# Kernel tuning notes

Measured on AMD Instinct MI355X. Metric: run time of the kernel, lower is better.

The kernel has to match this reference:

```python
import jax, jax.numpy as jnp
import numpy as np

ANCHOR_RADIUS = 5.0


def setup_inputs() -> dict:
    key = jax.random.key(0)
    k1, k2, k3 = jax.random.split(key, 3)
    B, N, E, S = 4, 1024, 32, 2
    embedding = jax.random.normal(k1, (B, N, E), dtype=jnp.float32)
    abs_coords = 10.0 * jax.random.normal(k2, (B, N, S), dtype=jnp.float32)
    patch_mask = jax.random.bernoulli(k3, 0.5, (B, N, N))  # bool [B,N,N]
    return {"embedding": embedding, "abs_coords": abs_coords, "patch_mask": patch_mask}


def reference(embedding, abs_coords, patch_mask):
    B, N, E = embedding.shape
    # pairwise coordinate and embedding differences
    coord_diff = abs_coords[:, :, None, :] - abs_coords[:, None, :, :]   # [B,N,N,2]
    diff = embedding[:, :, None, :] - embedding[:, None, :, :]           # [B,N,N,E]
    diff = diff.at[..., :2].add(coord_diff)
    ssq = jnp.sum(diff * diff, axis=-1)                                   # [B,N,N]
    # safe sqrt: zero grad at zero distance (matches torch norm subgradient)
    dist = jnp.where(ssq == 0, 0.0, jnp.sqrt(jnp.where(ssq == 0, 1.0, ssq)))
    sim = 1.0 - jax.nn.sigmoid(dist * 5.0 / ANCHOR_RADIUS - 5.0)          # [B,N,N]

    # negatives: sim with positive-pair mask and diagonal set to -inf
    eye = jnp.eye(N, dtype=bool)
    neg_mask = patch_mask | eye
    neg_masked = jnp.where(neg_mask, -jnp.inf, sim)                       # [B,N,N]
    lse_neg = jax.scipy.special.logsumexp(neg_masked, axis=-1)            # [B,N]

    # For each positive pair (b,i,j) with patch_mask[b,i,j]:
    #   logits = [sim[b,i,j], neg_masked[b,i,:]] ; CE target=0 ->
    #   loss_contrib = logaddexp(sim[b,i,j], lse_neg[b,i]) - sim[b,i,j]
    lse_tot = jnp.logaddexp(sim, lse_neg[:, :, None])                     # [B,N,N]
    loss = jnp.sum(jnp.where(patch_mask, lse_tot - sim, 0.0))
    return loss
```

## Files before the change

kernel.cpp:

```cpp
#include <hip/hip_runtime.h>

#define BBATCH 4
#define NN 1024
#define EE 32
#define NROW (BBATCH * NN)

typedef short v8s __attribute__((ext_vector_type(8)));
typedef float v4f __attribute__((ext_vector_type(4)));

#define WS_NRM  (NROW * EE * 2)
#define WS_SUM  (WS_NRM + NROW * 4)
#define WS_PART (WS_SUM + NROW * 4)

__device__ __forceinline__ unsigned short f32_to_bf16(float v) {
    unsigned u = __builtin_bit_cast(unsigned, v);
    u += 0x7fffu + ((u >> 16) & 1u);
    return (unsigned short)(u >> 16);
}

__global__ __launch_bounds__(256) void prep_kernel(
    const float* __restrict__ emb, const float* __restrict__ coords,
    unsigned short* __restrict__ yh, float* __restrict__ nrm)
{
    const int idx = blockIdx.x * 256 + threadIdx.x;
    const int g = idx >> 5, e = idx & 31;
    float v = emb[idx];
    if (e < 2) v += coords[g * 2 + e];
    yh[idx] = f32_to_bf16(v);
    float s = v * v;
    #pragma unroll
    for (int off = 16; off > 0; off >>= 1) s += __shfl_xor(s, off, 32);
    if (e == 0) nrm[g] = s;
}

__global__ __launch_bounds__(256) void passA_kernel(
    const unsigned short* __restrict__ yh, const float* __restrict__ nrm,
    const int* __restrict__ mask, float* __restrict__ sums)
{
    const int bid = blockIdx.x;
    const int jg = bid & 3;
    const int is = (bid >> 2) & 63;
    const int b  = bid >> 8;
    const int tid  = threadIdx.x;
    const int wave = tid >> 6, lane = tid & 63;
    const int m = lane & 15, q = lane >> 4;

    const int i0 = is * 16;
    const int rb = b * NN;
    const v8s af = *(const v8s*)(yh + (size_t)(rb + i0 + m) * EE + q * 8);
    float ni[4];
    #pragma unroll
    for (int r = 0; r < 4; ++r) ni[r] = nrm[rb + i0 + q * 4 + r];

    const int jbase = jg * 256 + wave * 64;
    float s[4] = {0.f, 0.f, 0.f, 0.f};

    #pragma unroll
    for (int t = 0; t < 4; ++t) {
        const int j0 = jbase + t * 16;
        const v8s bf = *(const v8s*)(yh + (size_t)(rb + j0 + m) * EE + q * 8);
        const float njv = nrm[rb + j0 + m];
        int mk[4];
        #pragma unroll
        for (int r = 0; r < 4; ++r)
            mk[r] = mask[((size_t)(rb + i0 + q * 4 + r) << 10) + j0 + m];
        v4f d = __builtin_amdgcn_mfma_f32_16x16x32_bf16(af, bf, (v4f){0,0,0,0}, 0, 0, 0);
        #pragma unroll
        for (int r = 0; r < 4; ++r) {
            float ssq  = fmaxf(ni[r] + njv - 2.f * d[r], 0.f);
            float dist = sqrtf(ssq);
            float sim  = 1.f / (1.f + __expf(dist - 5.f));
            bool negm  = (mk[r] != 0) || (i0 + q * 4 + r == j0 + m);
            s[r] += negm ? 0.f : __expf(sim);
        }
    }
    #pragma unroll
    for (int r = 0; r < 4; ++r) {
        float v = s[r];
        #pragma unroll
        for (int off = 8; off > 0; off >>= 1) v += __shfl_down(v, off, 16);
        if (m == 0) atomicAdd(&sums[rb + i0 + q * 4 + r], v);
    }
}

__global__ __launch_bounds__(256) void passB_kernel(
    const unsigned short* __restrict__ yh, const float* __restrict__ nrm,
    const int* __restrict__ mask, const float* __restrict__ sums,
    float* __restrict__ part)
{
    const int bid = blockIdx.x;
    const int jg = bid & 3;
    const int is = (bid >> 2) & 63;
    const int b  = bid >> 8;
    const int tid  = threadIdx.x;
    const int wave = tid >> 6, lane = tid & 63;
    const int m = lane & 15, q = lane >> 4;

    const int i0 = is * 16;
    const int rb = b * NN;
    const v8s af = *(const v8s*)(yh + (size_t)(rb + i0 + m) * EE + q * 8);
    float ni[4], tot[4];
    #pragma unroll
    for (int r = 0; r < 4; ++r) {
        ni[r]  = nrm[rb + i0 + q * 4 + r];
        tot[r] = sums[rb + i0 + q * 4 + r];
    }

    const int jbase = jg * 256 + wave * 64;
    float acc = 0.f;

    #pragma unroll
    for (int t = 0; t < 4; ++t) {
        const int j0 = jbase + t * 16;
        const v8s bf = *(const v8s*)(yh + (size_t)(rb + j0 + m) * EE + q * 8);
        const float njv = nrm[rb + j0 + m];
        int mk[4];
        #pragma unroll
        for (int r = 0; r < 4; ++r)
            mk[r] = mask[((size_t)(rb + i0 + q * 4 + r) << 10) + j0 + m];
        v4f d = __builtin_amdgcn_mfma_f32_16x16x32_bf16(af, bf, (v4f){0,0,0,0}, 0, 0, 0);
        #pragma unroll
        for (int r = 0; r < 4; ++r) {
            float ssq  = fmaxf(ni[r] + njv - 2.f * d[r], 0.f);
            float dist = sqrtf(ssq);
            float sim  = 1.f / (1.f + __expf(dist - 5.f));
            float term = __logf(fmaf(tot[r], __expf(-sim), 1.f));
            acc += (mk[r] != 0) ? term : 0.f;
        }
    }

    __shared__ float wred[4];
    #pragma unroll
    for (int off = 32; off > 0; off >>= 1) acc += __shfl_down(acc, off, 64);
    if (lane == 0) wred[wave] = acc;
    __syncthreads();
    if (tid == 0) part[bid] = wred[0] + wred[1] + wred[2] + wred[3];
}

__global__ __launch_bounds__(256) void reduce_kernel(
    const float* __restrict__ part, float* __restrict__ out)
{
    const int tid = threadIdx.x;
    float s = part[tid] + part[tid + 256] + part[tid + 512] + part[tid + 768];
    #pragma unroll
    for (int off = 32; off > 0; off >>= 1) s += __shfl_down(s, off, 64);
    __shared__ float w[4];
    if ((tid & 63) == 0) w[tid >> 6] = s;
    __syncthreads();
    if (tid == 0) out[0] = w[0] + w[1] + w[2] + w[3];
}

extern "C" void kernel_launch(void* const* d_in, const int* in_sizes, int n_in,
                              void* d_out, int out_size, void* d_ws, size_t ws_size,
                              hipStream_t stream) {
    const float* emb    = (const float*)d_in[0];
    const float* coords = (const float*)d_in[1];
    const int*   mask   = (const int*)d_in[2];

    char* ws = (char*)d_ws;
    unsigned short* yh   = (unsigned short*)ws;
    float*          nrm  = (float*)(ws + WS_NRM);
    float*          sums = (float*)(ws + WS_SUM);
    float*          part = (float*)(ws + WS_PART);

    hipMemsetAsync(sums, 0, NROW * sizeof(float), stream);
    prep_kernel  <<<(NROW * EE) / 256, 256, 0, stream>>>(emb, coords, yh, nrm);
    passA_kernel <<<1024, 256, 0, stream>>>(yh, nrm, mask, sums);
    passB_kernel <<<1024, 256, 0, stream>>>(yh, nrm, mask, sums, part);
    reduce_kernel<<<1, 256, 0, stream>>>(part, (float*)d_out);
}
```

Baseline: 86.88 us.

## Fuse two-pass contrastive loss into one kernel with in-block row sums

Merges passA, passB and the final reduction into one kernel. Each 1024-thread block now owns 16 full rows across all 1024 columns, so the negative-sum for each row is finished in shared memory. The similarity values and mask bits stay in registers for the second phase. This removes the second pass over the mask and MFMA recompute, the per-row atomics and memset, and two kernel launches. The cost is far fewer blocks (256), higher register pressure, and a float atomic on the output that makes the summation order nondeterministic.

```diff
diff --git a/kernel.cpp b/kernel.cpp
--- a/kernel.cpp
+++ b/kernel.cpp
@@ -9,8 +9,6 @@
 typedef float v4f __attribute__((ext_vector_type(4)));
 
 #define WS_NRM  (NROW * EE * 2)
-#define WS_SUM  (WS_NRM + NROW * 4)
-#define WS_PART (WS_SUM + NROW * 4)
 
 __device__ __forceinline__ unsigned short f32_to_bf16(float v) {
     unsigned u = __builtin_bit_cast(unsigned, v);
@@ -33,14 +31,13 @@
     if (e == 0) nrm[g] = s;
 }
 
-__global__ __launch_bounds__(256) void passA_kernel(
+__global__ __launch_bounds__(1024) void fused_kernel(
     const unsigned short* __restrict__ yh, const float* __restrict__ nrm,
-    const int* __restrict__ mask, float* __restrict__ sums)
+    const int* __restrict__ mask, float* __restrict__ out)
 {
     const int bid = blockIdx.x;
-    const int jg = bid & 3;
-    const int is = (bid >> 2) & 63;
-    const int b  = bid >> 8;
+    const int is = bid & 63;
+    const int b  = bid >> 6;
     const int tid  = threadIdx.x;
     const int wave = tid >> 6, lane = tid & 63;
     const int m = lane & 15, q = lane >> 4;
@@ -52,8 +49,10 @@
     #pragma unroll
     for (int r = 0; r < 4; ++r) ni[r] = nrm[rb + i0 + q * 4 + r];
 
-    const int jbase = jg * 256 + wave * 64;
-    float s[4] = {0.f, 0.f, 0.f, 0.f};
+    const int jbase = wave * 64;
+    float    sim[4][4];
+    float    s[4] = {0.f, 0.f, 0.f, 0.f};
+    unsigned mbits = 0u;
 
     #pragma unroll
     for (int t = 0; t < 4; ++t) {
@@ -69,85 +68,54 @@
         for (int r = 0; r < 4; ++r) {
             float ssq  = fmaxf(ni[r] + njv - 2.f * d[r], 0.f);
             float dist = sqrtf(ssq);
-            float sim  = 1.f / (1.f + __expf(dist - 5.f));
+            float sm   = 1.f / (1.f + __expf(dist - 5.f));
+            sim[t][r]  = sm;
             bool negm  = (mk[r] != 0) || (i0 + q * 4 + r == j0 + m);
-            s[r] += negm ? 0.f : __expf(sim);
+            s[r] += negm ? 0.f : __expf(sm);
+            if (mk[r] != 0) mbits |= 1u << (t * 4 + r);
         }
     }
+
+    __shared__ float sums_w[16][16];
+    __shared__ float total_s[16];
+    __shared__ float wred[16];
     #pragma unroll
     for (int r = 0; r < 4; ++r) {
         float v = s[r];
         #pragma unroll
         for (int off = 8; off > 0; off >>= 1) v += __shfl_down(v, off, 16);
-        if (m == 0) atomicAdd(&sums[rb + i0 + q * 4 + r], v);
+        if (m == 0) sums_w[wave][q * 4 + r] = v;
     }
-}
+    __syncthreads();
+    if (tid < 16) {
+        float tot = 0.f;
+        #pragma unroll
+        for (int w = 0; w < 16; ++w) tot += sums_w[w][tid];
+        total_s[tid] = tot;
+    }
+    __syncthreads();
 
-__global__ __launch_bounds__(256) void passB_kernel(
-    const unsigned short* __restrict__ yh, const float* __restrict__ nrm,
-    const int* __restrict__ mask, const float* __restrict__ sums,
-    float* __restrict__ part)
-{
-    const int bid = blockIdx.x;
-    const int jg = bid & 3;
-    const int is = (bid >> 2) & 63;
-    const int b  = bid >> 8;
-    const int tid  = threadIdx.x;
-    const int wave = tid >> 6, lane = tid & 63;
-    const int m = lane & 15, q = lane >> 4;
-
-    const int i0 = is * 16;
-    const int rb = b * NN;
-    const v8s af = *(const v8s*)(yh + (size_t)(rb + i0 + m) * EE + q * 8);
-    float ni[4], tot[4];
+    float tot[4];
     #pragma unroll
-    for (int r = 0; r < 4; ++r) {
-        ni[r]  = nrm[rb + i0 + q * 4 + r];
-        tot[r] = sums[rb + i0 + q * 4 + r];
-    }
-
-    const int jbase = jg * 256 + wave * 64;
+    for (int r = 0; r < 4; ++r) tot[r] = total_s[q * 4 + r];
     float acc = 0.f;
-
     #pragma unroll
-    for (int t = 0; t < 4; ++t) {
-        const int j0 = jbase + t * 16;
-        const v8s bf = *(const v8s*)(yh + (size_t)(rb + j0 + m) * EE + q * 8);
-        const float njv = nrm[rb + j0 + m];
-        int mk[4];
+    for (int t = 0; t < 4; ++t)
         #pragma unroll
         for (int r = 0; r < 4; ++r)
-            mk[r] = mask[((size_t)(rb + i0 + q * 4 + r) << 10) + j0 + m];
-        v4f d = __builtin_amdgcn_mfma_f32_16x16x32_bf16(af, bf, (v4f){0,0,0,0}, 0, 0, 0);
-        #pragma unroll
-        for (int r = 0; r < 4; ++r) {
-            float ssq  = fmaxf(ni[r] + njv - 2.f * d[r], 0.f);
-            float dist = sqrtf(ssq);
-            float sim  = 1.f / (1.f + __expf(dist - 5.f));
-            float term = __logf(fmaf(tot[r], __expf(-sim), 1.f));
-            acc += (mk[r] != 0) ? term : 0.f;
-        }
-    }
+            if ((mbits >> (t * 4 + r)) & 1u)
+                acc += __logf(fmaf(tot[r], __expf(-sim[t][r]), 1.f));
 
-    __shared__ float wred[4];
     #pragma unroll
     for (int off = 32; off > 0; off >>= 1) acc += __shfl_down(acc, off, 64);
     if (lane == 0) wred[wave] = acc;
     __syncthreads();
-    if (tid == 0) part[bid] = wred[0] + wred[1] + wred[2] + wred[3];
-}
-
-__global__ __launch_bounds__(256) void reduce_kernel(
-    const float* __restrict__ part, float* __restrict__ out)
-{
-    const int tid = threadIdx.x;
-    float s = part[tid] + part[tid + 256] + part[tid + 512] + part[tid + 768];
-    #pragma unroll
-    for (int off = 32; off > 0; off >>= 1) s += __shfl_down(s, off, 64);
-    __shared__ float w[4];
-    if ((tid & 63) == 0) w[tid >> 6] = s;
-    __syncthreads();
-    if (tid == 0) out[0] = w[0] + w[1] + w[2] + w[3];
+    if (tid == 0) {
+        float a = 0.f;
+        #pragma unroll
+        for (int w = 0; w < 16; ++w) a += wred[w];
+        atomicAdd(out, a);
+    }
 }
 
 extern "C" void kernel_launch(void* const* d_in, const int* in_sizes, int n_in,
@@ -156,16 +124,13 @@
     const float* emb    = (const float*)d_in[0];
     const float* coords = (const float*)d_in[1];
     const int*   mask   = (const int*)d_in[2];
+    float*       out    = (float*)d_out;
 
     char* ws = (char*)d_ws;
-    unsigned short* yh   = (unsigned short*)ws;
-    float*          nrm  = (float*)(ws + WS_NRM);
-    float*          sums = (float*)(ws + WS_SUM);
-    float*          part = (float*)(ws + WS_PART);
+    unsigned short* yh  = (unsigned short*)ws;
+    float*          nrm = (float*)(ws + WS_NRM);
 
-    hipMemsetAsync(sums, 0, NROW * sizeof(float), stream);
-    prep_kernel  <<<(NROW * EE) / 256, 256, 0, stream>>>(emb, coords, yh, nrm);
-    passA_kernel <<<1024, 256, 0, stream>>>(yh, nrm, mask, sums);
-    passB_kernel <<<1024, 256, 0, stream>>>(yh, nrm, mask, sums, part);
-    reduce_kernel<<<1, 256, 0, stream>>>(part, (float*)d_out);
+    hipMemsetAsync(out, 0, sizeof(float), stream);
+    prep_kernel <<<(NROW * EE) / 256, 256, 0, stream>>>(emb, coords, yh, nrm);
+    fused_kernel<<<BBATCH * (NN / 16), 1024, 0, stream>>>(yh, nrm, mask, out);
 }
```

Result: faster. 80.94 us (-6.8%).
